# Kernel tuning notes

Hardware: AMD Instinct MI355X
Metric: run time of the kernel (lower is better)

Reference implementation:

```python
import jax, jax.numpy as jnp
import numpy as np

N_NODES = 50000
N_EDGES = 500000
CLIP_DIM = 512   # openai/clip-vit-base-patch32 projection_dim
HIDDEN = 512
NUM_CLASSES = 100


def setup_inputs() -> dict:
    key = jax.random.key(0)
    ks = jax.random.split(key, 8)
    x = jax.random.normal(ks[0], (N_NODES, CLIP_DIM), dtype=jnp.float32)
    edge_index = jax.random.randint(ks[1], (2, N_EDGES), 0, N_NODES)
    W1 = jax.random.normal(ks[2], (HIDDEN, CLIP_DIM), dtype=jnp.float32) / np.sqrt(CLIP_DIM)
    b1 = jnp.zeros((HIDDEN,), dtype=jnp.float32)
    W2 = jax.random.normal(ks[3], (HIDDEN, HIDDEN), dtype=jnp.float32) / np.sqrt(HIDDEN)
    b2 = jnp.zeros((HIDDEN,), dtype=jnp.float32)
    Wc = jax.random.normal(ks[4], (NUM_CLASSES, HIDDEN), dtype=jnp.float32) / np.sqrt(HIDDEN)
    bc = jnp.zeros((NUM_CLASSES,), dtype=jnp.float32)
    return {"x": x, "edge_index": edge_index, "W1": W1, "b1": b1,
            "W2": W2, "b2": b2, "Wc": Wc, "bc": bc}


def _gcn_conv(h, W, b, src, dst, coef, n_nodes):
    # PyG GCNConv: transform, then normalized scatter-add aggregation, then bias.
    h = h @ W.T                                   # [N, out]
    msg = h[src] * coef[:, None]                  # [E+N, out] gathered messages
    out = jax.ops.segment_sum(msg, dst, num_segments=n_nodes)
    return out + b


def reference(x, edge_index, W1, b1, W2, b2, Wc, bc):
    n = x.shape[0]
    loop = jnp.arange(n, dtype=edge_index.dtype)
    src = jnp.concatenate([edge_index[0], loop])  # add self-loops (GCN default)
    dst = jnp.concatenate([edge_index[1], loop])
    # symmetric normalization deg^-1/2 on both endpoints (unit edge weights)
    deg = jax.ops.segment_sum(jnp.ones_like(src, dtype=x.dtype), dst, num_segments=n)
    norm = jax.lax.rsqrt(deg)                     # deg >= 1 due to self-loops
    coef = norm[src] * norm[dst]

    h = _gcn_conv(x, W1, b1, src, dst, coef, n)
    h = jax.nn.relu(h)
    # dropout(p=0.2) is identity in eval mode
    h = _gcn_conv(h, W2, b2, src, dst, coef, n)
    h = jax.nn.relu(h)
    return h @ Wc.T + bc                          # [N, num_classes]
```

## Files before the change

### kernel.cpp

```cpp
#include <hip/hip_runtime.h>

#define HIDDEN 512
#define BLK_ELEMS (64 * 128 * 8)

typedef __attribute__((ext_vector_type(8))) short short8;
typedef __attribute__((ext_vector_type(4))) float f32x4;

__device__ __forceinline__ unsigned short f2bf(float f) {
    unsigned u = __float_as_uint(f);
    unsigned r = (u + 0x7FFFu + ((u >> 16) & 1u)) >> 16;
    return (unsigned short)r;
}
__device__ __forceinline__ float bf2f(unsigned short h) {
    return __uint_as_float(((unsigned)h) << 16);
}

__device__ __forceinline__ void load_lds16(const unsigned short* g, unsigned short* l) {
    __builtin_amdgcn_global_load_lds(
        (const __attribute__((address_space(1))) unsigned int*)(g),
        (__attribute__((address_space(3))) unsigned int*)(l), 16, 0, 0);
}

__device__ __forceinline__ void acc8(uint4 v, float cf, float* a) {
    a[0] = fmaf(cf, bf2f((unsigned short)(v.x & 0xFFFF)), a[0]);
    a[1] = fmaf(cf, bf2f((unsigned short)(v.x >> 16)),    a[1]);
    a[2] = fmaf(cf, bf2f((unsigned short)(v.y & 0xFFFF)), a[2]);
    a[3] = fmaf(cf, bf2f((unsigned short)(v.y >> 16)),    a[3]);
    a[4] = fmaf(cf, bf2f((unsigned short)(v.z & 0xFFFF)), a[4]);
    a[5] = fmaf(cf, bf2f((unsigned short)(v.z >> 16)),    a[5]);
    a[6] = fmaf(cf, bf2f((unsigned short)(v.w & 0xFFFF)), a[6]);
    a[7] = fmaf(cf, bf2f((unsigned short)(v.w >> 16)),    a[7]);
}


__global__ void count_kernel(const int* __restrict__ dst, int* __restrict__ cnt, int E) {
    int e = blockIdx.x * 256 + threadIdx.x;
    if (e < E) atomicAdd(&cnt[dst[e]], 1);
}

__global__ __launch_bounds__(256)
void bsum_norm_kernel(const int* __restrict__ cnt, float* __restrict__ norm,
                      int* __restrict__ bsums, int n) {
    __shared__ int red[256];
    int tid = threadIdx.x;
    int i = blockIdx.x * 256 + tid;
    int v = 0;
    if (i < n) {
        v = cnt[i];
        norm[i] = rsqrtf((float)(v + 1));
    }
    red[tid] = v;
    __syncthreads();
    #pragma unroll
    for (int off = 128; off > 0; off >>= 1) {
        if (tid < off) red[tid] += red[tid + off];
        __syncthreads();
    }
    if (tid == 0) bsums[blockIdx.x] = red[0];
}

__global__ __launch_bounds__(256)
void bscan_kernel(const int* __restrict__ bsums, int* __restrict__ boffs,
                  int* __restrict__ rowptr_n, int nb) {
    __shared__ int buf[256];
    int tid = threadIdx.x;
    int v = (tid < nb) ? bsums[tid] : 0;
    buf[tid] = v;
    __syncthreads();
    #pragma unroll
    for (int off = 1; off < 256; off <<= 1) {
        int t = (tid >= off) ? buf[tid - off] : 0;
        __syncthreads();
        buf[tid] += t;
        __syncthreads();
    }
    if (tid < nb) boffs[tid] = buf[tid] - v;
    if (tid == 255) rowptr_n[0] = buf[255];
}

__global__ __launch_bounds__(256)
void scan_final_kernel(const int* __restrict__ cnt, const int* __restrict__ boffs,
                       int* __restrict__ rowptr, int* __restrict__ cursor, int n) {
    __shared__ int buf[256];
    int tid = threadIdx.x;
    int i = blockIdx.x * 256 + tid;
    int v = (i < n) ? cnt[i] : 0;
    buf[tid] = v;
    __syncthreads();
    #pragma unroll
    for (int off = 1; off < 256; off <<= 1) {
        int t = (tid >= off) ? buf[tid - off] : 0;
        __syncthreads();
        buf[tid] += t;
        __syncthreads();
    }
    if (i < n) {
        int ex = boffs[blockIdx.x] + buf[tid] - v;
        rowptr[i] = ex;
        cursor[i] = ex;
    }
}

__global__ void fill_kernel(const int* __restrict__ src, const int* __restrict__ dst,
                            const float* __restrict__ norm, int* __restrict__ cursor,
                            int2* __restrict__ epair, int E) {
    int e = blockIdx.x * 256 + threadIdx.x;
    if (e < E) {
        int s = src[e], d = dst[e];
        float cf = norm[s] * norm[d];
        int p = atomicAdd(&cursor[d], 1);
        epair[p] = make_int2(s, __float_as_int(cf));
    }
}


__device__ __forceinline__ void cast_chunk(const float* __restrict__ src,
                                           unsigned short* __restrict__ dst,
                                           int rows, int o) {
    int blk = o >> 13;
    int rem = o & 8191;
    int g = rem >> 7;
    int m = rem & 127;
    int row = blk * 128 + m;
    short8 v;
    if (row < rows) {
        const float* p = src + (size_t)row * HIDDEN + g * 8;
        float4 f0 = *(const float4*)p;
        float4 f1 = *(const float4*)(p + 4);
        v[0] = (short)f2bf(f0.x); v[1] = (short)f2bf(f0.y);
        v[2] = (short)f2bf(f0.z); v[3] = (short)f2bf(f0.w);
        v[4] = (short)f2bf(f1.x); v[5] = (short)f2bf(f1.y);
        v[6] = (short)f2bf(f1.z); v[7] = (short)f2bf(f1.w);
    } else {
        v = (short8)0;
    }
    *(short8*)(dst + (size_t)o * 8) = v;
}

__global__ __launch_bounds__(256)
void cast_tiled_kernel(const float* __restrict__ src, unsigned short* __restrict__ dst,
                       int rows, int total_chunks) {
    int o = blockIdx.x * 256 + threadIdx.x;
    if (o >= total_chunks) return;
    cast_chunk(src, dst, rows, o);
}

__global__ __launch_bounds__(256)
void cast_w3_kernel(const float* __restrict__ W1, const float* __restrict__ W2,
                    const float* __restrict__ Wc,
                    unsigned short* __restrict__ W1t, unsigned short* __restrict__ W2t,
                    unsigned short* __restrict__ Wct, int NC) {
    int o = blockIdx.x * 256 + threadIdx.x;
    if (o < 32768) {
        cast_chunk(W1, W1t, HIDDEN, o);
    } else if (o < 65536) {
        cast_chunk(W2, W2t, HIDDEN, o - 32768);
    } else if (o < 73728) {
        cast_chunk(Wc, Wct, NC, o - 65536);
    }
}


template<int MODE, int SWIZ>
__global__ __launch_bounds__(256)
void gemm_bf16(const unsigned short* __restrict__ At, const unsigned short* __restrict__ Bt,
               const float* __restrict__ bias, void* __restrict__ Cout,
               int M, int NC, int NB) {
    __shared__ __align__(16) unsigned short As[8 * 128 * 8];
    __shared__ __align__(16) unsigned short Bs[8 * 128 * 8];

    int mb, nb;
    if (SWIZ) {
        int bid = blockIdx.x;
        int p = bid & 7;
        int s = bid >> 3;
        nb = s & 3;
        mb = (s >> 2) * 8 + p;
        if (mb >= NB) return;
    } else {
        mb = blockIdx.x;
        nb = blockIdx.y;
    }

    const int tid = threadIdx.x;
    const int wid = tid >> 6;
    const int lane = tid & 63;
    const int wm = wid & 1, wn = wid >> 1;
    const int lm = lane & 15;
    const int lq = lane >> 4;

    const unsigned short* Ab = At + (size_t)mb * BLK_ELEMS;
    const unsigned short* Bb = Bt + (size_t)nb * BLK_ELEMS;

    f32x4 acc[4][4];
    #pragma unroll
    for (int i = 0; i < 4; ++i)
        #pragma unroll
        for (int j = 0; j < 4; ++j) acc[i][j] = (f32x4)0.f;

    for (int kt = 0; kt < 8; ++kt) {
        __syncthreads();
        const unsigned short* ga = Ab + kt * (8 * 1024);
        const unsigned short* gb = Bb + kt * (8 * 1024);
        #pragma unroll
        for (int i = 0; i < 4; ++i) {
            int off = (tid + i * 256) * 8;
            load_lds16(ga + off, As + off);
            load_lds16(gb + off, Bs + off);
        }
        __syncthreads();
        #pragma unroll
        for (int ks = 0; ks < 2; ++ks) {
            int g = ks * 4 + lq;
            int base = g * 1024 + lm * 8;
            short8 af[4], bfr[4];
            #pragma unroll
            for (int mt = 0; mt < 4; ++mt)
                af[mt] = *(const short8*)&As[base + (wm * 64 + mt * 16) * 8];
            #pragma unroll
            for (int nt = 0; nt < 4; ++nt)
                bfr[nt] = *(const short8*)&Bs[base + (wn * 64 + nt * 16) * 8];
            #pragma unroll
            for (int mt = 0; mt < 4; ++mt)
                #pragma unroll
                for (int nt = 0; nt < 4; ++nt)
                    acc[mt][nt] = __builtin_amdgcn_mfma_f32_16x16x32_bf16(
                        af[mt], bfr[nt], acc[mt][nt], 0, 0, 0);
        }
    }

    #pragma unroll
    for (int mt = 0; mt < 4; ++mt) {
        #pragma unroll
        for (int nt = 0; nt < 4; ++nt) {
            int col = nb * 128 + wn * 64 + nt * 16 + lm;
            f32x4 v = acc[mt][nt];
            #pragma unroll
            for (int r = 0; r < 4; ++r) {
                int row = mb * 128 + wm * 64 + mt * 16 + lq * 4 + r;
                if (row < M) {
                    if (MODE == 0) {
                        ((unsigned short*)Cout)[(size_t)row * HIDDEN + col] = f2bf(v[r]);
                    } else {
                        if (col < NC)
                            ((float*)Cout)[(size_t)row * NC + col] = v[r] + bias[col];
                    }
                }
            }
        }
    }
}


__global__ __launch_bounds__(256)
void aggregate_kernel(const unsigned short* __restrict__ h, const int* __restrict__ rowptr,
                      const int2* __restrict__ epair, const float* __restrict__ norm,
                      const float* __restrict__ bias, unsigned short* __restrict__ out_t,
                      int N) {
    const int wave = threadIdx.x >> 6;
    const int lane = threadIdx.x & 63;
    const int node = blockIdx.x * 4 + wave;
    if (node >= N) return;
    const uint4* h4 = (const uint4*)h;
    const int c = lane;

    float a[8];
    {
        uint4 sv = h4[(size_t)node * 64 + c];
        float nv = norm[node];
        float invd = nv * nv;
        a[0] = a[1] = a[2] = a[3] = a[4] = a[5] = a[6] = a[7] = 0.f;
        acc8(sv, invd, a);
    }

    int beg = rowptr[node], end = rowptr[node + 1];
    int j = beg;
    for (; j + 4 <= end; j += 4) {
        int2 p0 = epair[j + 0];
        int2 p1 = epair[j + 1];
        int2 p2 = epair[j + 2];
        int2 p3 = epair[j + 3];
        uint4 v0 = h4[(size_t)p0.x * 64 + c];
        uint4 v1 = h4[(size_t)p1.x * 64 + c];
        uint4 v2 = h4[(size_t)p2.x * 64 + c];
        uint4 v3 = h4[(size_t)p3.x * 64 + c];
        acc8(v0, __int_as_float(p0.y), a);
        acc8(v1, __int_as_float(p1.y), a);
        acc8(v2, __int_as_float(p2.y), a);
        acc8(v3, __int_as_float(p3.y), a);
    }
    for (; j < end; ++j) {
        int2 p = epair[j];
        uint4 v = h4[(size_t)p.x * 64 + c];
        acc8(v, __int_as_float(p.y), a);
    }

    const float4 b0 = *(const float4*)(bias + c * 8);
    const float4 b1 = *(const float4*)(bias + c * 8 + 4);
    a[0] = fmaxf(a[0] + b0.x, 0.f); a[1] = fmaxf(a[1] + b0.y, 0.f);
    a[2] = fmaxf(a[2] + b0.z, 0.f); a[3] = fmaxf(a[3] + b0.w, 0.f);
    a[4] = fmaxf(a[4] + b1.x, 0.f); a[5] = fmaxf(a[5] + b1.y, 0.f);
    a[6] = fmaxf(a[6] + b1.z, 0.f); a[7] = fmaxf(a[7] + b1.w, 0.f);

    size_t off = (size_t)(node >> 7) * BLK_ELEMS + (size_t)c * 1024 + (node & 127) * 8;
    uint4 o;
    o.x = (unsigned)f2bf(a[0]) | ((unsigned)f2bf(a[1]) << 16);
    o.y = (unsigned)f2bf(a[2]) | ((unsigned)f2bf(a[3]) << 16);
    o.z = (unsigned)f2bf(a[4]) | ((unsigned)f2bf(a[5]) << 16);
    o.w = (unsigned)f2bf(a[6]) | ((unsigned)f2bf(a[7]) << 16);
    *(uint4*)(out_t + off) = o;
}


extern "C" void kernel_launch(void* const* d_in, const int* in_sizes, int n_in,
                              void* d_out, int out_size, void* d_ws, size_t ws_size,
                              hipStream_t stream) {
    const float* x  = (const float*)d_in[0];
    const int*   ei = (const int*)d_in[1];
    const float* W1 = (const float*)d_in[2];
    const float* b1 = (const float*)d_in[3];
    const float* W2 = (const float*)d_in[4];
    const float* b2 = (const float*)d_in[5];
    const float* Wc = (const float*)d_in[6];
    const float* bc = (const float*)d_in[7];

    const int N  = in_sizes[0] / HIDDEN;
    const int E  = in_sizes[1] / 2;
    const int NC = in_sizes[6] / HIDDEN;
    const int NB = (N + 127) / 128;
    const int NSB = (N + 255) / 256;

    const int* src = ei;
    const int* dst = ei + E;

    char* ws = (char*)d_ws;
    int*   cnt    = (int*)(ws);
    int*   rowptr = (int*)(ws + (256 << 10));
    int*   cursor = (int*)(ws + (512 << 10));
    float* normv  = (float*)(ws + (768 << 10));
    int*   bsums  = (int*)(ws + (968 << 10));
    int*   boffs  = (int*)(ws + (990 << 10));
    int2*  epair  = (int2*)(ws + (1ull << 20));
    unsigned short* W1t = (unsigned short*)(ws + (6ull << 20));
    unsigned short* W2t = (unsigned short*)(ws + (6ull << 20) + (512 << 10));
    unsigned short* Wct = (unsigned short*)(ws + (7ull << 20));
    unsigned short* bufA = (unsigned short*)(ws + (16ull << 20));
    unsigned short* bufB = (unsigned short*)(ws + (80ull << 20));
    unsigned short* hbuf = (unsigned short*)(ws + (144ull << 20));

    hipMemsetAsync(cnt, 0, N * sizeof(int), stream);
    count_kernel<<<(E + 255) / 256, 256, 0, stream>>>(dst, cnt, E);
    bsum_norm_kernel<<<NSB, 256, 0, stream>>>(cnt, normv, bsums, N);
    bscan_kernel<<<1, 256, 0, stream>>>(bsums, boffs, rowptr + N, NSB);
    scan_final_kernel<<<NSB, 256, 0, stream>>>(cnt, boffs, rowptr, cursor, N);
    fill_kernel<<<(E + 255) / 256, 256, 0, stream>>>(src, dst, normv, cursor, epair, E);

    int xchunks = NB * 8192;
    cast_tiled_kernel<<<(xchunks + 255) / 256, 256, 0, stream>>>(x, bufA, N, xchunks);
    cast_w3_kernel<<<288, 256, 0, stream>>>(W1, W2, Wc, W1t, W2t, Wct, NC);

    const int gswz = 8 * 4 * ((NB + 7) / 8);
    gemm_bf16<0, 1><<<gswz, 256, 0, stream>>>(bufA, W1t, nullptr, hbuf, N, HIDDEN, NB);
    aggregate_kernel<<<(N + 3) / 4, 256, 0, stream>>>(hbuf, rowptr, epair, normv, b1, bufB, N);
    gemm_bf16<0, 1><<<gswz, 256, 0, stream>>>(bufB, W2t, nullptr, hbuf, N, HIDDEN, NB);
    aggregate_kernel<<<(N + 3) / 4, 256, 0, stream>>>(hbuf, rowptr, epair, normv, b2, bufA, N);
    dim3 gc(NB, 1);
    gemm_bf16<1, 0><<<gc, 256, 0, stream>>>(bufA, Wct, bc, d_out, N, NC, NB);
}
```

Baseline: 536.6 us.

## Co-launch independent preprocessing and GEMM kernels, widen aggregate edge loads

Merges independent stages into combined launches, split by block index: edge counting with the x cast, degree reduction with the weight casts, and CSR fill with the first GEMM. This cuts the number of launches and lets small, latency-bound kernels overlap with bandwidth or compute work. The aggregate loop now reads edge pairs as 16-byte int4 after an alignment peel and processes 8 neighbours per iteration, giving more gathers in flight. The risks are higher register and LDS use in the fused kernels, since their branches carry the GEMM's shared buffers, and uneven block workloads.

Result: faster. 514.1 us (-4.2%).

```diff
diff --git a/kernel.cpp b/kernel.cpp
--- a/kernel.cpp
+++ b/kernel.cpp
@@ -30,87 +30,6 @@
     a[5] = fmaf(cf, bf2f((unsigned short)(v.z >> 16)),    a[5]);
     a[6] = fmaf(cf, bf2f((unsigned short)(v.w & 0xFFFF)), a[6]);
     a[7] = fmaf(cf, bf2f((unsigned short)(v.w >> 16)),    a[7]);
-}
-
-
-__global__ void count_kernel(const int* __restrict__ dst, int* __restrict__ cnt, int E) {
-    int e = blockIdx.x * 256 + threadIdx.x;
-    if (e < E) atomicAdd(&cnt[dst[e]], 1);
-}
-
-__global__ __launch_bounds__(256)
-void bsum_norm_kernel(const int* __restrict__ cnt, float* __restrict__ norm,
-                      int* __restrict__ bsums, int n) {
-    __shared__ int red[256];
-    int tid = threadIdx.x;
-    int i = blockIdx.x * 256 + tid;
-    int v = 0;
-    if (i < n) {
-        v = cnt[i];
-        norm[i] = rsqrtf((float)(v + 1));
-    }
-    red[tid] = v;
-    __syncthreads();
-    #pragma unroll
-    for (int off = 128; off > 0; off >>= 1) {
-        if (tid < off) red[tid] += red[tid + off];
-        __syncthreads();
-    }
-    if (tid == 0) bsums[blockIdx.x] = red[0];
-}
-
-__global__ __launch_bounds__(256)
-void bscan_kernel(const int* __restrict__ bsums, int* __restrict__ boffs,
-                  int* __restrict__ rowptr_n, int nb) {
-    __shared__ int buf[256];
-    int tid = threadIdx.x;
-    int v = (tid < nb) ? bsums[tid] : 0;
-    buf[tid] = v;
-    __syncthreads();
-    #pragma unroll
-    for (int off = 1; off < 256; off <<= 1) {
-        int t = (tid >= off) ? buf[tid - off] : 0;
-        __syncthreads();
-        buf[tid] += t;
-        __syncthreads();
-    }
-    if (tid < nb) boffs[tid] = buf[tid] - v;
-    if (tid == 255) rowptr_n[0] = buf[255];
-}
-
-__global__ __launch_bounds__(256)
-void scan_final_kernel(const int* __restrict__ cnt, const int* __restrict__ boffs,
-                       int* __restrict__ rowptr, int* __restrict__ cursor, int n) {
-    __shared__ int buf[256];
-    int tid = threadIdx.x;
-    int i = blockIdx.x * 256 + tid;
-    int v = (i < n) ? cnt[i] : 0;
-    buf[tid] = v;
-    __syncthreads();
-    #pragma unroll
-    for (int off = 1; off < 256; off <<= 1) {
-        int t = (tid >= off) ? buf[tid - off] : 0;
-        __syncthreads();
-        buf[tid] += t;
-        __syncthreads();
-    }
-    if (i < n) {
-        int ex = boffs[blockIdx.x] + buf[tid] - v;
-        rowptr[i] = ex;
-        cursor[i] = ex;
-    }
-}
-
-__global__ void fill_kernel(const int* __restrict__ src, const int* __restrict__ dst,
-                            const float* __restrict__ norm, int* __restrict__ cursor,
-                            int2* __restrict__ epair, int E) {
-    int e = blockIdx.x * 256 + threadIdx.x;
-    if (e < E) {
-        int s = src[e], d = dst[e];
-        float cf = norm[s] * norm[d];
-        int p = atomicAdd(&cursor[d], 1);
-        epair[p] = make_int2(s, __float_as_int(cf));
-    }
 }
 
 
@@ -137,50 +56,109 @@
     *(short8*)(dst + (size_t)o * 8) = v;
 }
 
-__global__ __launch_bounds__(256)
-void cast_tiled_kernel(const float* __restrict__ src, unsigned short* __restrict__ dst,
-                       int rows, int total_chunks) {
-    int o = blockIdx.x * 256 + threadIdx.x;
-    if (o >= total_chunks) return;
-    cast_chunk(src, dst, rows, o);
-}
-
-__global__ __launch_bounds__(256)
-void cast_w3_kernel(const float* __restrict__ W1, const float* __restrict__ W2,
-                    const float* __restrict__ Wc,
-                    unsigned short* __restrict__ W1t, unsigned short* __restrict__ W2t,
-                    unsigned short* __restrict__ Wct, int NC) {
-    int o = blockIdx.x * 256 + threadIdx.x;
-    if (o < 32768) {
-        cast_chunk(W1, W1t, HIDDEN, o);
-    } else if (o < 65536) {
-        cast_chunk(W2, W2t, HIDDEN, o - 32768);
-    } else if (o < 73728) {
-        cast_chunk(Wc, Wct, NC, o - 65536);
-    }
-}
-
-
-template<int MODE, int SWIZ>
-__global__ __launch_bounds__(256)
-void gemm_bf16(const unsigned short* __restrict__ At, const unsigned short* __restrict__ Bt,
-               const float* __restrict__ bias, void* __restrict__ Cout,
-               int M, int NC, int NB) {
+
+__global__ __launch_bounds__(256)
+void fused_count_castx(const int* __restrict__ dstv, int* __restrict__ cnt, int E, int countB,
+                       const float* __restrict__ x, unsigned short* __restrict__ bufA,
+                       int rows, int xchunks) {
+    int b = blockIdx.x;
+    if (b < countB) {
+        int e = b * 256 + threadIdx.x;
+        if (e < E) atomicAdd(&cnt[dstv[e]], 1);
+    } else {
+        int o = (b - countB) * 256 + threadIdx.x;
+        if (o < xchunks) cast_chunk(x, bufA, rows, o);
+    }
+}
+
+
+__global__ __launch_bounds__(256)
+void fused_bsum_castw(const int* __restrict__ cnt, float* __restrict__ norm,
+                      int* __restrict__ bsums, int n, int NSB,
+                      const float* __restrict__ W1, const float* __restrict__ W2,
+                      const float* __restrict__ Wc,
+                      unsigned short* __restrict__ W1t, unsigned short* __restrict__ W2t,
+                      unsigned short* __restrict__ Wct, int NC) {
+    __shared__ int red[256];
+    int tid = threadIdx.x;
+    if ((int)blockIdx.x < NSB) {
+        int i = blockIdx.x * 256 + tid;
+        int v = 0;
+        if (i < n) {
+            v = cnt[i];
+            norm[i] = rsqrtf((float)(v + 1));
+        }
+        red[tid] = v;
+        __syncthreads();
+        #pragma unroll
+        for (int off = 128; off > 0; off >>= 1) {
+            if (tid < off) red[tid] += red[tid + off];
+            __syncthreads();
+        }
+        if (tid == 0) bsums[blockIdx.x] = red[0];
+    } else {
+        int o = ((int)blockIdx.x - NSB) * 256 + tid;
+        if (o < 32768) {
+            cast_chunk(W1, W1t, HIDDEN, o);
+        } else if (o < 65536) {
+            cast_chunk(W2, W2t, HIDDEN, o - 32768);
+        } else if (o < 73728) {
+            cast_chunk(Wc, Wct, NC, o - 65536);
+        }
+    }
+}
+
+__global__ __launch_bounds__(256)
+void bscan_kernel(const int* __restrict__ bsums, int* __restrict__ boffs,
+                  int* __restrict__ rowptr_n, int nb) {
+    __shared__ int buf[256];
+    int tid = threadIdx.x;
+    int v = (tid < nb) ? bsums[tid] : 0;
+    buf[tid] = v;
+    __syncthreads();
+    #pragma unroll
+    for (int off = 1; off < 256; off <<= 1) {
+        int t = (tid >= off) ? buf[tid - off] : 0;
+        __syncthreads();
+        buf[tid] += t;
+        __syncthreads();
+    }
+    if (tid < nb) boffs[tid] = buf[tid] - v;
+    if (tid == 255) rowptr_n[0] = buf[255];
+}
+
+__global__ __launch_bounds__(256)
+void scan_final_kernel(const int* __restrict__ cnt, const int* __restrict__ boffs,
+                       int* __restrict__ rowptr, int* __restrict__ cursor, int n) {
+    __shared__ int buf[256];
+    int tid = threadIdx.x;
+    int i = blockIdx.x * 256 + tid;
+    int v = (i < n) ? cnt[i] : 0;
+    buf[tid] = v;
+    __syncthreads();
+    #pragma unroll
+    for (int off = 1; off < 256; off <<= 1) {
+        int t = (tid >= off) ? buf[tid - off] : 0;
+        __syncthreads();
+        buf[tid] += t;
+        __syncthreads();
+    }
+    if (i < n) {
+        int ex = boffs[blockIdx.x] + buf[tid] - v;
+        rowptr[i] = ex;
+        cursor[i] = ex;
+    }
+}
+
+
+template<int MODE>
+__device__ __forceinline__ void gemm_body(const unsigned short* __restrict__ At,
+                                          const unsigned short* __restrict__ Bt,
+                                          const float* __restrict__ bias,
+                                          void* __restrict__ Cout,
+                                          int M, int NC, int mb, int nb) {
     __shared__ __align__(16) unsigned short As[8 * 128 * 8];
     __shared__ __align__(16) unsigned short Bs[8 * 128 * 8];
-
-    int mb, nb;
-    if (SWIZ) {
-        int bid = blockIdx.x;
-        int p = bid & 7;
-        int s = bid >> 3;
-        nb = s & 3;
-        mb = (s >> 2) * 8 + p;
-        if (mb >= NB) return;
-    } else {
-        mb = blockIdx.x;
-        nb = blockIdx.y;
-    }
 
     const int tid = threadIdx.x;
     const int wid = tid >> 6;
@@ -251,6 +229,55 @@
     }
 }
 
+__device__ __forceinline__ bool swz_decode(int bid, int NB, int& mb, int& nb) {
+    int p = bid & 7;
+    int s = bid >> 3;
+    nb = s & 3;
+    mb = (s >> 2) * 8 + p;
+    return mb < NB;
+}
+
+template<int MODE>
+__global__ __launch_bounds__(256)
+void gemm_swz(const unsigned short* __restrict__ At, const unsigned short* __restrict__ Bt,
+              const float* __restrict__ bias, void* __restrict__ Cout,
+              int M, int NC, int NB) {
+    int mb, nb;
+    if (!swz_decode(blockIdx.x, NB, mb, nb)) return;
+    gemm_body<MODE>(At, Bt, bias, Cout, M, NC, mb, nb);
+}
+
+template<int MODE>
+__global__ __launch_bounds__(256)
+void gemm_plain(const unsigned short* __restrict__ At, const unsigned short* __restrict__ Bt,
+                const float* __restrict__ bias, void* __restrict__ Cout,
+                int M, int NC) {
+    gemm_body<MODE>(At, Bt, bias, Cout, M, NC, blockIdx.x, blockIdx.y);
+}
+
+
+__global__ __launch_bounds__(256)
+void fused_fill_gemm1(const int* __restrict__ src, const int* __restrict__ dstv,
+                      const float* __restrict__ norm, int* __restrict__ cursor,
+                      int2* __restrict__ epair, int E, int fillB,
+                      const unsigned short* __restrict__ At, const unsigned short* __restrict__ Bt,
+                      void* __restrict__ Cout, int M, int NB) {
+    int b = blockIdx.x;
+    if (b < fillB) {
+        int e = b * 256 + threadIdx.x;
+        if (e < E) {
+            int s = src[e], d = dstv[e];
+            float cf = norm[s] * norm[d];
+            int p = atomicAdd(&cursor[d], 1);
+            epair[p] = make_int2(s, __float_as_int(cf));
+        }
+    } else {
+        int mb, nb;
+        if (swz_decode(b - fillB, NB, mb, nb))
+            gemm_body<0>(At, Bt, nullptr, Cout, M, HIDDEN, mb, nb);
+    }
+}
+
 
 __global__ __launch_bounds__(256)
 void aggregate_kernel(const unsigned short* __restrict__ h, const int* __restrict__ rowptr,
@@ -275,19 +302,33 @@
 
     int beg = rowptr[node], end = rowptr[node + 1];
     int j = beg;
-    for (; j + 4 <= end; j += 4) {
-        int2 p0 = epair[j + 0];
-        int2 p1 = epair[j + 1];
-        int2 p2 = epair[j + 2];
-        int2 p3 = epair[j + 3];
-        uint4 v0 = h4[(size_t)p0.x * 64 + c];
-        uint4 v1 = h4[(size_t)p1.x * 64 + c];
-        uint4 v2 = h4[(size_t)p2.x * 64 + c];
-        uint4 v3 = h4[(size_t)p3.x * 64 + c];
-        acc8(v0, __int_as_float(p0.y), a);
-        acc8(v1, __int_as_float(p1.y), a);
-        acc8(v2, __int_as_float(p2.y), a);
-        acc8(v3, __int_as_float(p3.y), a);
+    if ((j & 1) && j < end) {
+        int2 p = epair[j];
+        uint4 v = h4[(size_t)p.x * 64 + c];
+        acc8(v, __int_as_float(p.y), a);
+        ++j;
+    }
+    for (; j + 8 <= end; j += 8) {
+        int4 q0 = *(const int4*)(epair + j);
+        int4 q1 = *(const int4*)(epair + j + 2);
+        int4 q2 = *(const int4*)(epair + j + 4);
+        int4 q3 = *(const int4*)(epair + j + 6);
+        uint4 v0 = h4[(size_t)q0.x * 64 + c];
+        uint4 v1 = h4[(size_t)q0.z * 64 + c];
+        uint4 v2 = h4[(size_t)q1.x * 64 + c];
+        uint4 v3 = h4[(size_t)q1.z * 64 + c];
+        uint4 v4 = h4[(size_t)q2.x * 64 + c];
+        uint4 v5 = h4[(size_t)q2.z * 64 + c];
+        uint4 v6 = h4[(size_t)q3.x * 64 + c];
+        uint4 v7 = h4[(size_t)q3.z * 64 + c];
+        acc8(v0, __int_as_float(q0.y), a);
+        acc8(v1, __int_as_float(q0.w), a);
+        acc8(v2, __int_as_float(q1.y), a);
+        acc8(v3, __int_as_float(q1.w), a);
+        acc8(v4, __int_as_float(q2.y), a);
+        acc8(v5, __int_as_float(q2.w), a);
+        acc8(v6, __int_as_float(q3.y), a);
+        acc8(v7, __int_as_float(q3.w), a);
     }
     for (; j < end; ++j) {
         int2 p = epair[j];
@@ -348,22 +389,23 @@
     unsigned short* bufB = (unsigned short*)(ws + (80ull << 20));
     unsigned short* hbuf = (unsigned short*)(ws + (144ull << 20));
 
+    const int countB = (E + 255) / 256;
+    const int xchunks = NB * 8192;
+    const int castxB = (xchunks + 255) / 256;
+    const int gemmB = 8 * 4 * ((NB + 7) / 8);
+
     hipMemsetAsync(cnt, 0, N * sizeof(int), stream);
-    count_kernel<<<(E + 255) / 256, 256, 0, stream>>>(dst, cnt, E);
-    bsum_norm_kernel<<<NSB, 256, 0, stream>>>(cnt, normv, bsums, N);
+    fused_count_castx<<<countB + castxB, 256, 0, stream>>>(dst, cnt, E, countB,
+                                                           x, bufA, N, xchunks);
+    fused_bsum_castw<<<NSB + 288, 256, 0, stream>>>(cnt, normv, bsums, N, NSB,
+                                                    W1, W2, Wc, W1t, W2t, Wct, NC);
     bscan_kernel<<<1, 256, 0, stream>>>(bsums, boffs, rowptr + N, NSB);
     scan_final_kernel<<<NSB, 256, 0, stream>>>(cnt, boffs, rowptr, cursor, N);
-    fill_kernel<<<(E + 255) / 256, 256, 0, stream>>>(src, dst, normv, cursor, epair, E);
-
-    int xchunks = NB * 8192;
-    cast_tiled_kernel<<<(xchunks + 255) / 256, 256, 0, stream>>>(x, bufA, N, xchunks);
-    cast_w3_kernel<<<288, 256, 0, stream>>>(W1, W2, Wc, W1t, W2t, Wct, NC);
-
-    const int gswz = 8 * 4 * ((NB + 7) / 8);
-    gemm_bf16<0, 1><<<gswz, 256, 0, stream>>>(bufA, W1t, nullptr, hbuf, N, HIDDEN, NB);
+    fused_fill_gemm1<<<countB + gemmB, 256, 0, stream>>>(src, dst, normv, cursor, epair,
+                                                         E, countB,
+                                                         bufA, W1t, hbuf, N, NB);
     aggregate_kernel<<<(N + 3) / 4, 256, 0, stream>>>(hbuf, rowptr, epair, normv, b1, bufB, N);
-    gemm_bf16<0, 1><<<gswz, 256, 0, stream>>>(bufB, W2t, nullptr, hbuf, N, HIDDEN, NB);
+    gemm_swz<0><<<gemmB, 256, 0, stream>>>(bufB, W2t, nullptr, hbuf, N, HIDDEN, NB);
     aggregate_kernel<<<(N + 3) / 4, 256, 0, stream>>>(hbuf, rowptr, epair, normv, b2, bufA, N);
-    dim3 gc(NB, 1);
-    gemm_bf16<1, 0><<<gc, 256, 0, stream>>>(bufA, Wct, bc, d_out, N, NC, NB);
-}
+    gemm_plain<1><<<dim3(NB, 1), 256, 0, stream>>>(bufA, Wct, bc, d_out, N, NC);
+}
```
